# Performance work log

Measured on AMD Instinct MI355X. Metric: run time of the kernel, lower is better.

Reference implementation:

```python
import jax, jax.numpy as jnp
import numpy as np

N = 131072      # total nodes across batched graphs
E = 524288      # total directed edges (avg degree 4, molecular graphs)
F_NODE = 64     # raw atom features
F_BOND = 16     # raw bond features
D = 128         # hidden width (hard-coded in the module)
H2 = 16
G = 4096        # number of graphs in the batch
DIM_OUT = 1


def _make_params(key):
    ks = iter(jax.random.split(key, 64))
    def w(shape, scale):
        return jax.random.normal(next(ks), shape, jnp.float32) * scale
    p = {"fc1_w": w((F_NODE, D), 0.1), "fc1_b": jnp.zeros((D,), jnp.float32)}
    for l in (1, 2, 3):
        p[f"gc{l}_wq"] = w((D, D), 0.05); p[f"gc{l}_bq"] = jnp.zeros((D,), jnp.float32)
        p[f"gc{l}_wk"] = w((D, D), 0.05); p[f"gc{l}_bk"] = jnp.zeros((D,), jnp.float32)
        p[f"gc{l}_wv"] = w((D, D), 0.05); p[f"gc{l}_bv"] = jnp.zeros((D,), jnp.float32)
        p[f"gc{l}_we"] = w((F_BOND, D), 0.05)   # PyG lin_edge has no bias
        p[f"gc{l}_ws"] = w((D, D), 0.05); p[f"gc{l}_bs"] = jnp.zeros((D,), jnp.float32)
    p["fc2_w"] = w((D, H2), 0.1); p["fc2_b"] = jnp.zeros((H2,), jnp.float32)
    p["fc3_w"] = w((H2, DIM_OUT), 0.1); p["fc3_b"] = jnp.zeros((DIM_OUT,), jnp.float32)
    return p


def setup_inputs() -> dict:
    key = jax.random.key(0)
    k1, k2, k3, k4, kp = jax.random.split(key, 5)
    inp = {
        "x": jax.random.normal(k1, (N, F_NODE), jnp.float32),
        "edge_index": jax.random.randint(k2, (2, E), 0, N),
        "edge_attr": jax.random.normal(k3, (E, F_BOND), jnp.float32),
        "batch": jnp.sort(jax.random.randint(k4, (N,), 0, G)),
    }
    inp.update(_make_params(kp))
    return inp


def _tconv(x, src, dst, edge_attr, wq, bq, wk, bk, wv, bv, we, ws, bs):
    # PyG TransformerConv, heads=1, concat=True, beta=False, root_weight=True
    n = x.shape[0]
    q = x @ wq + bq                                   # [N,D]
    k = x @ wk + bk                                   # [N,D]
    v = x @ wv + bv                                   # [N,D]
    e = edge_attr @ we                                # [E,D] edge projection
    kj = k[src] + e                                   # key_j + edge
    vj = v[src] + e                                   # value_j + edge
    alpha = jnp.sum(q[dst] * kj, axis=-1) / jnp.sqrt(jnp.float32(D))   # [E]
    # segment softmax over incoming edges of each dst node
    amax = jax.ops.segment_max(alpha, dst, num_segments=n)
    ex = jnp.exp(alpha - amax[dst])
    denom = jax.ops.segment_sum(ex, dst, num_segments=n)
    w = ex / denom[dst]                               # [E]
    agg = jax.ops.segment_sum(vj * w[:, None], dst, num_segments=n)    # scatter-add
    return agg + x @ ws + bs                          # skip / root weight


def reference(x, edge_index, edge_attr, batch,
              fc1_w, fc1_b,
              gc1_wq, gc1_bq, gc1_wk, gc1_bk, gc1_wv, gc1_bv, gc1_we, gc1_ws, gc1_bs,
              gc2_wq, gc2_bq, gc2_wk, gc2_bk, gc2_wv, gc2_bv, gc2_we, gc2_ws, gc2_bs,
              gc3_wq, gc3_bq, gc3_wk, gc3_bk, gc3_wv, gc3_bv, gc3_we, gc3_ws, gc3_bs,
              fc2_w, fc2_b, fc3_w, fc3_b):
    src, dst = edge_index[0], edge_index[1]
    h = x @ fc1_w + fc1_b
    layers = [
        (gc1_wq, gc1_bq, gc1_wk, gc1_bk, gc1_wv, gc1_bv, gc1_we, gc1_ws, gc1_bs),
        (gc2_wq, gc2_bq, gc2_wk, gc2_bk, gc2_wv, gc2_bv, gc2_we, gc2_ws, gc2_bs),
        (gc3_wq, gc3_bq, gc3_wk, gc3_bk, gc3_wv, gc3_bv, gc3_we, gc3_ws, gc3_bs),
    ]
    for p in layers:
        h = jax.nn.relu(_tconv(h, src, dst, edge_attr, *p))
    # global mean pool over graph ids
    cnt = jax.ops.segment_sum(jnp.ones((h.shape[0],), h.dtype), batch, num_segments=G)
    hg = jax.ops.segment_sum(h, batch, num_segments=G) / jnp.maximum(cnt, 1.0)[:, None]
    h = jax.nn.relu(hg @ fc2_w + fc2_b)
    return h @ fc3_w + fc3_b                          # [G, DIM_OUT]
```

## Files before the change

kernel.cpp:

```cpp
#include <hip/hip_runtime.h>
#include <hip/hip_fp16.h>


#define D 128

typedef _Float16 half8 __attribute__((ext_vector_type(8)));
typedef float f32x4 __attribute__((ext_vector_type(4)));

__global__ __launch_bounds__(256) void hist_kernel(const int* __restrict__ dst,
                                                   int* __restrict__ counts, int e) {
  int i = blockIdx.x * 256 + threadIdx.x;
  if (i < e) atomicAdd(&counts[dst[i]], 1);
}

__global__ __launch_bounds__(256) void scan_a_kernel(const int* __restrict__ counts,
                                                     int* __restrict__ incl,
                                                     int* __restrict__ bsum) {
  int gid = blockIdx.x * 256 + threadIdx.x;
  int lane = threadIdx.x & 63, wid = threadIdx.x >> 6;
  int v = counts[gid];
  int s = v;
  #pragma unroll
  for (int off = 1; off < 64; off <<= 1) {
    int t = __shfl_up(s, off, 64);
    if (lane >= off) s += t;
  }
  __shared__ int wsum[4];
  if (lane == 63) wsum[wid] = s;
  __syncthreads();
  #pragma unroll
  for (int w = 0; w < 3; ++w)
    if (wid > w) s += wsum[w];
  incl[gid] = s;
  if (threadIdx.x == 255) bsum[blockIdx.x] = s;
}

__global__ __launch_bounds__(512) void scan_b_kernel(int* __restrict__ bs) {
  int tid = threadIdx.x;
  int lane = tid & 63, wid = tid >> 6;
  int v = bs[tid];
  int s = v;
  #pragma unroll
  for (int off = 1; off < 64; off <<= 1) {
    int t = __shfl_up(s, off, 64);
    if (lane >= off) s += t;
  }
  __shared__ int wsum[8];
  if (lane == 63) wsum[wid] = s;
  __syncthreads();
  #pragma unroll
  for (int w = 0; w < 7; ++w)
    if (wid > w) s += wsum[w];
  bs[tid] = s - v;
}

__global__ __launch_bounds__(256) void scan_c_kernel(const int* __restrict__ incl,
                                                     const int* __restrict__ counts,
                                                     const int* __restrict__ bsum,
                                                     int* __restrict__ offs, int n, int e) {
  int gid = blockIdx.x * 256 + threadIdx.x;
  if (gid < n) offs[gid] = incl[gid] - counts[gid] + bsum[blockIdx.x];
  if (gid == 0) offs[n] = e;
}

__global__ __launch_bounds__(256) void scatter_kernel(const int* __restrict__ srcs,
                                                      const int* __restrict__ dsts,
                                                      const int* __restrict__ offs,
                                                      int* __restrict__ cursor,
                                                      int* __restrict__ csr_src,
                                                      int* __restrict__ csr_eid, int e) {
  int i = blockIdx.x * 256 + threadIdx.x;
  if (i >= e) return;
  int d = dsts[i];
  int slot = atomicAdd(&cursor[d], 1);
  int p = offs[d] + slot;
  csr_src[p] = srcs[i];
  csr_eid[p] = i;
}

__global__ __launch_bounds__(256) void sort_kernel(const int* __restrict__ offs,
                                                   int* __restrict__ eid,
                                                   int* __restrict__ srcs, int n) {
  int i = blockIdx.x * 256 + threadIdx.x;
  if (i >= n) return;
  int b = offs[i], e = offs[i + 1];
  for (int p = b + 1; p < e; ++p) {
    int ke = eid[p], ks = srcs[p];
    int q = p - 1;
    while (q >= b && eid[q] > ke) {
      eid[q + 1] = eid[q]; srcs[q + 1] = srcs[q]; --q;
    }
    eid[q + 1] = ke; srcs[q + 1] = ks;
  }
}

__global__ __launch_bounds__(256) void convw_kernel(const float* __restrict__ W,
                                                    __half* __restrict__ out,
                                                    int ncols, int K) {
  int idx = blockIdx.x * 256 + threadIdx.x;
  if (idx >= ncols * K) return;
  int n = idx / K, kk = idx - n * K;
  out[idx] = __float2half(W[(size_t)kk * ncols + n]);
}

__global__ __launch_bounds__(256) void bcat_kernel(const float* __restrict__ bq,
                                                   const float* __restrict__ bk,
                                                   const float* __restrict__ bv,
                                                   const float* __restrict__ bs,
                                                   float* __restrict__ out) {
  int j = blockIdx.x * 256 + threadIdx.x;
  if (j >= 512) return;
  const float* src = (j < 128) ? bq : (j < 256) ? bk : (j < 384) ? bv : bs;
  out[j] = src[j & 127];
}

__device__ inline void store4h(__half* p, float4 v) {
  __half2 h01 = __floats2half2_rn(v.x, v.y);
  __half2 h23 = __floats2half2_rn(v.z, v.w);
  uint2 u;
  u.x = *(unsigned int*)&h01;
  u.y = *(unsigned int*)&h23;
  *(uint2*)p = u;
}

template <int K, int NCT, bool QKVS>
__global__ __launch_bounds__(256) void mfma_gemm_kernel(
    const float* in, const __half* __restrict__ Wt, const float* __restrict__ bias,
    __half* __restrict__ oq, __half* __restrict__ ok, __half* __restrict__ ov,
    float* os) {
  constexpr int WST = K + 8;
  __shared__ alignas(16) __half Wc[128 * WST];
  const int tid = threadIdx.x;
  const int w = tid >> 6, l = tid & 63;
  const int lo = l & 15, hi = l >> 4;
  const size_t row = (size_t)blockIdx.x * 64 + w * 16 + lo;

  half8 af[K / 32];
  #pragma unroll
  for (int s = 0; s < K / 32; ++s) {
    const float* sp = in + row * K + s * 32 + hi * 8;
    float4 f0 = *(const float4*)sp;
    float4 f1 = *(const float4*)(sp + 4);
    half8 a;
    a[0] = (_Float16)f0.x; a[1] = (_Float16)f0.y; a[2] = (_Float16)f0.z; a[3] = (_Float16)f0.w;
    a[4] = (_Float16)f1.x; a[5] = (_Float16)f1.y; a[6] = (_Float16)f1.z; a[7] = (_Float16)f1.w;
    af[s] = a;
  }

  #pragma unroll 1
  for (int ch = 0; ch < NCT / 8; ++ch) {
    __syncthreads();
    #pragma unroll
    for (int i = 0; i < 128 * K / 8 / 256; ++i) {
      int idx = i * 256 + tid;
      int col = idx / (K / 8), kk = (idx % (K / 8)) * 8;
      *(uint4*)&Wc[col * WST + kk] =
          *(const uint4*)(Wt + (size_t)(ch * 128 + col) * K + kk);
    }
    __syncthreads();

    #pragma unroll
    for (int t = 0; t < 8; ++t) {
      f32x4 c = {0.f, 0.f, 0.f, 0.f};
      #pragma unroll
      for (int s = 0; s < K / 32; ++s) {
        half8 bf = *(const half8*)&Wc[(t * 16 + lo) * WST + s * 32 + hi * 8];
        c = __builtin_amdgcn_mfma_f32_16x16x32_f16(bf, af[s], c, 0, 0, 0);
      }
      const int col0 = ch * 128 + t * 16 + hi * 4;
      float4 b4 = *(const float4*)(bias + col0);
      float4 o;
      o.x = c[0] + b4.x; o.y = c[1] + b4.y; o.z = c[2] + b4.z; o.w = c[3] + b4.w;
      if (QKVS) {
        const int mid = col0 >> 7, cc = col0 & 127;
        if (mid == 0)      store4h(oq + row * 128 + cc, o);
        else if (mid == 1) store4h(ok + row * 128 + cc, o);
        else if (mid == 2) store4h(ov + row * 128 + cc, o);
        else               *(float4*)(os + row * 128 + cc) = o;
      } else {
        *(float4*)(os + row * 128 + col0) = o;
      }
    }
  }
}

__global__ __launch_bounds__(256) void node_kernel(
    const __half* __restrict__ q, const __half* __restrict__ k, const __half* __restrict__ v,
    float* __restrict__ h, const float* __restrict__ edge_attr,
    const float* __restrict__ we,
    const int* __restrict__ offs, const int* __restrict__ csr_src,
    const int* __restrict__ csr_eid) {
  const int wid = threadIdx.x >> 6, lane = threadIdx.x & 63;
  const int node = __builtin_amdgcn_readfirstlane(blockIdx.x * 4 + wid);
  const int c0 = lane * 2;
  const float inv_sqrt_d = 0.08838834764831845f;

  float2 wreg[16];
  #pragma unroll
  for (int f = 0; f < 16; ++f)
    wreg[f] = *(const float2*)(we + f * D + c0);

  float2 qv = __half22float2(((const __half2*)q)[(size_t)node * 64 + lane]);
  qv.x *= inv_sqrt_d; qv.y *= inv_sqrt_d;
  float2 sv = *(const float2*)(h + (size_t)node * D + c0);

  const int eb = offs[node], ee = offs[node + 1];
  float m = -3.0e38f, den = 0.f, accx = 0.f, accy = 0.f;

  float4 a0n = {0,0,0,0}, a1n = {0,0,0,0}, a2n = {0,0,0,0}, a3n = {0,0,0,0};
  float2 kvn = {0.f, 0.f}, vvn = {0.f, 0.f};
  int p = eb;
  if (p < ee) {
    int src = __builtin_amdgcn_readfirstlane(csr_src[p]);
    int eid = __builtin_amdgcn_readfirstlane(csr_eid[p]);
    const float* ea = edge_attr + (size_t)eid * 16;
    a0n = *(const float4*)(ea + 0);  a1n = *(const float4*)(ea + 4);
    a2n = *(const float4*)(ea + 8);  a3n = *(const float4*)(ea + 12);
    kvn = __half22float2(((const __half2*)k)[(size_t)src * 64 + lane]);
    vvn = __half22float2(((const __half2*)v)[(size_t)src * 64 + lane]);
  }
  while (p < ee) {
    float4 a0 = a0n, a1 = a1n, a2 = a2n, a3 = a3n;
    float2 kv = kvn, vv = vvn;
    ++p;
    if (p < ee) {
      int src = __builtin_amdgcn_readfirstlane(csr_src[p]);
      int eid = __builtin_amdgcn_readfirstlane(csr_eid[p]);
      const float* ea = edge_attr + (size_t)eid * 16;
      a0n = *(const float4*)(ea + 0);  a1n = *(const float4*)(ea + 4);
      a2n = *(const float4*)(ea + 8);  a3n = *(const float4*)(ea + 12);
      kvn = __half22float2(((const __half2*)k)[(size_t)src * 64 + lane]);
      vvn = __half22float2(((const __half2*)v)[(size_t)src * 64 + lane]);
    }
    float ea16[16] = {a0.x, a0.y, a0.z, a0.w, a1.x, a1.y, a1.z, a1.w,
                      a2.x, a2.y, a2.z, a2.w, a3.x, a3.y, a3.z, a3.w};
    float evx = 0.f, evy = 0.f;
    #pragma unroll
    for (int f = 0; f < 16; ++f) {
      evx += ea16[f] * wreg[f].x;
      evy += ea16[f] * wreg[f].y;
    }
    float pa = qv.x * (kv.x + evx) + qv.y * (kv.y + evy);
    #pragma unroll
    for (int off = 32; off > 0; off >>= 1) pa += __shfl_xor(pa, off, 64);
    float vjx = vv.x + evx, vjy = vv.y + evy;
    float mn = fmaxf(m, pa);
    float esc = __expf(m - mn);
    float ew = __expf(pa - mn);
    den = den * esc + ew;
    accx = accx * esc + ew * vjx;
    accy = accy * esc + ew * vjy;
    m = mn;
  }
  if (den > 0.f) {
    sv.x += accx / den;
    sv.y += accy / den;
  }
  sv.x = fmaxf(sv.x, 0.f);
  sv.y = fmaxf(sv.y, 0.f);
  *(float2*)(h + (size_t)node * D + c0) = sv;
}

__global__ __launch_bounds__(64) void pool_kernel(const float* __restrict__ h,
                                                  const int* __restrict__ batch,
                                                  float* __restrict__ hg,
                                                  float* __restrict__ cnt, int n) {
  int base = blockIdx.x * 128;
  int lane = threadIdx.x;
  float2 acc = {0.f, 0.f};
  float run = 0.f;
  int cur = batch[base];
  for (int i = 0; i < 128; ++i) {
    int node = base + i;
    int g = batch[node];
    if (g != cur) {
      atomicAdd(&hg[(size_t)cur * D + 2 * lane], acc.x);
      atomicAdd(&hg[(size_t)cur * D + 2 * lane + 1], acc.y);
      if (lane == 0) atomicAdd(&cnt[cur], run);
      acc.x = acc.y = 0.f; run = 0.f; cur = g;
    }
    float2 hv = *(const float2*)(h + (size_t)node * D + 2 * lane);
    acc.x += hv.x; acc.y += hv.y; run += 1.f;
  }
  atomicAdd(&hg[(size_t)cur * D + 2 * lane], acc.x);
  atomicAdd(&hg[(size_t)cur * D + 2 * lane + 1], acc.y);
  if (lane == 0) atomicAdd(&cnt[cur], run);
}

__global__ __launch_bounds__(256) void head_kernel(const float* __restrict__ hg,
                                                   const float* __restrict__ cnt,
                                                   const float* __restrict__ w2,
                                                   const float* __restrict__ b2,
                                                   const float* __restrict__ w3,
                                                   const float* __restrict__ b3,
                                                   float* __restrict__ out) {
  __shared__ float w2s[128 * 16];
  __shared__ float rowb[4][128];
  for (int i = threadIdx.x; i < (128 * 16) / 4; i += 256)
    ((float4*)w2s)[i] = ((const float4*)w2)[i];
  int wid = threadIdx.x >> 6, lane = threadIdx.x & 63;
  int g = blockIdx.x * 4 + wid;
  float inv = 1.0f / fmaxf(cnt[g], 1.0f);
  rowb[wid][lane] = hg[(size_t)g * D + lane] * inv;
  rowb[wid][lane + 64] = hg[(size_t)g * D + 64 + lane] * inv;
  __syncthreads();
  float t = 0.f;
  if (lane < 16) {
    float a = b2[lane];
    for (int d = 0; d < 128; ++d) a += rowb[wid][d] * w2s[d * 16 + lane];
    t = fmaxf(a, 0.f) * w3[lane];
  }
  #pragma unroll
  for (int off = 8; off > 0; off >>= 1) t += __shfl_xor(t, off, 64);
  if (lane == 0) out[g] = t + b3[0];
}

extern "C" void kernel_launch(void* const* d_in, const int* in_sizes, int n_in,
                              void* d_out, int out_size, void* d_ws, size_t ws_size,
                              hipStream_t stream) {
  const float* x = (const float*)d_in[0];
  const int* eidx = (const int*)d_in[1];
  const float* eattr = (const float*)d_in[2];
  const int* batch = (const int*)d_in[3];
  const float* fc1_w = (const float*)d_in[4];
  const float* fc1_b = (const float*)d_in[5];
  const float* WQ[3] = {(const float*)d_in[6], (const float*)d_in[15], (const float*)d_in[24]};
  const float* BQ[3] = {(const float*)d_in[7], (const float*)d_in[16], (const float*)d_in[25]};
  const float* WK[3] = {(const float*)d_in[8], (const float*)d_in[17], (const float*)d_in[26]};
  const float* BK[3] = {(const float*)d_in[9], (const float*)d_in[18], (const float*)d_in[27]};
  const float* WV[3] = {(const float*)d_in[10], (const float*)d_in[19], (const float*)d_in[28]};
  const float* BV[3] = {(const float*)d_in[11], (const float*)d_in[20], (const float*)d_in[29]};
  const float* WE[3] = {(const float*)d_in[12], (const float*)d_in[21], (const float*)d_in[30]};
  const float* WS[3] = {(const float*)d_in[13], (const float*)d_in[22], (const float*)d_in[31]};
  const float* BS[3] = {(const float*)d_in[14], (const float*)d_in[23], (const float*)d_in[32]};
  const float* fc2_w = (const float*)d_in[33];
  const float* fc2_b = (const float*)d_in[34];
  const float* fc3_w = (const float*)d_in[35];
  const float* fc3_b = (const float*)d_in[36];

  const int N = in_sizes[0] / 64;
  const int E = in_sizes[1] / 2;
  const int G = out_size;
  const int* srcs = eidx;
  const int* dsts = eidx + E;
  const size_t ND = (size_t)N * D;

  char* base = (char*)d_ws;
  size_t off = 0;
  auto alloc = [&](size_t bytes) {
    void* p = base + off;
    off = (off + bytes + 255) & ~(size_t)255;
    return p;
  };
  float* hg = (float*)alloc((size_t)G * D * 4);
  float* cntf = (float*)alloc((size_t)G * 4);
  int* counts = (int*)alloc((size_t)N * 4);
  int* cursor = (int*)alloc((size_t)N * 4);
  size_t zero_bytes = (size_t)G * D * 4 + (size_t)G * 4 + 2 * (size_t)N * 4;
  int* incl = (int*)alloc((size_t)N * 4);
  int* offs = (int*)alloc((size_t)(N + 4) * 4);
  int* bsum = (int*)alloc(512 * 4);
  int* csr_src = (int*)alloc((size_t)E * 4);
  int* csr_eid = (int*)alloc((size_t)E * 4);
  float* h = (float*)alloc(ND * 4);
  __half* q = (__half*)alloc(ND * 2);
  __half* k = (__half*)alloc(ND * 2);
  __half* v = (__half*)alloc(ND * 2);
  __half* Wt[3];
  float* bc[3];
  for (int l = 0; l < 3; ++l) {
    Wt[l] = (__half*)alloc(512 * 128 * 2);
    bc[l] = (float*)alloc(512 * 4);
  }
  __half* fc1t = (__half*)alloc(128 * 64 * 2);
  if (off > ws_size) return;

  hipMemsetAsync(hg, 0, zero_bytes, stream);

  for (int l = 0; l < 3; ++l) {
    convw_kernel<<<64, 256, 0, stream>>>(WQ[l], Wt[l] + 0 * 16384, 128, 128);
    convw_kernel<<<64, 256, 0, stream>>>(WK[l], Wt[l] + 1 * 16384, 128, 128);
    convw_kernel<<<64, 256, 0, stream>>>(WV[l], Wt[l] + 2 * 16384, 128, 128);
    convw_kernel<<<64, 256, 0, stream>>>(WS[l], Wt[l] + 3 * 16384, 128, 128);
    bcat_kernel<<<2, 256, 0, stream>>>(BQ[l], BK[l], BV[l], BS[l], bc[l]);
  }
  convw_kernel<<<32, 256, 0, stream>>>(fc1_w, fc1t, 128, 64);

  hist_kernel<<<E / 256, 256, 0, stream>>>(dsts, counts, E);
  scan_a_kernel<<<N / 256, 256, 0, stream>>>(counts, incl, bsum);
  scan_b_kernel<<<1, 512, 0, stream>>>(bsum);
  scan_c_kernel<<<N / 256, 256, 0, stream>>>(incl, counts, bsum, offs, N, E);
  scatter_kernel<<<E / 256, 256, 0, stream>>>(srcs, dsts, offs, cursor, csr_src, csr_eid, E);
  sort_kernel<<<N / 256, 256, 0, stream>>>(offs, csr_eid, csr_src, N);

  mfma_gemm_kernel<64, 8, false><<<N / 64, 256, 0, stream>>>(
      x, fc1t, fc1_b, nullptr, nullptr, nullptr, h);

  for (int l = 0; l < 3; ++l) {
    mfma_gemm_kernel<128, 32, true><<<N / 64, 256, 0, stream>>>(
        h, Wt[l], bc[l], q, k, v, h);
    node_kernel<<<N / 4, 256, 0, stream>>>(q, k, v, h, eattr, WE[l],
                                           offs, csr_src, csr_eid);
  }

  pool_kernel<<<N / 128, 64, 0, stream>>>(h, batch, hg, cntf, N);
  head_kernel<<<G / 4, 256, 0, stream>>>(hg, cntf, fc2_w, fc2_b, fc3_w, fc3_b, (float*)d_out);
}
```

Baseline: 654.7 us.

## Fold edge projection into query-side precompute and defer edge value projection

Result: slower. 705.7 us (+7.8%).

```diff
diff --git a/kernel.cpp b/kernel.cpp
--- a/kernel.cpp
+++ b/kernel.cpp
@@ -103,6 +103,25 @@
   out[idx] = __float2half(W[(size_t)kk * ncols + n]);
 }
 
+__global__ __launch_bounds__(256) void convwe_kernel(const float* __restrict__ we,
+                                                     const float* __restrict__ Wq,
+                                                     const float* __restrict__ bq,
+                                                     __half* __restrict__ outW,
+                                                     float* __restrict__ outB) {
+  int idx = blockIdx.x * 256 + threadIdx.x;
+  if (idx < 2048) {
+    int f = idx >> 7, kk = idx & 127;
+    float s = 0.f;
+    for (int d = 0; d < 128; ++d) s += we[f * 128 + d] * Wq[kk * 128 + d];
+    outW[f * 128 + kk] = __float2half(s);
+  } else if (idx < 2064) {
+    int f = idx - 2048;
+    float s = 0.f;
+    for (int d = 0; d < 128; ++d) s += we[f * 128 + d] * bq[d];
+    outB[f] = s;
+  }
+}
+
 __global__ __launch_bounds__(256) void bcat_kernel(const float* __restrict__ bq,
                                                    const float* __restrict__ bk,
                                                    const float* __restrict__ bv,
@@ -127,7 +146,7 @@
 __global__ __launch_bounds__(256) void mfma_gemm_kernel(
     const float* in, const __half* __restrict__ Wt, const float* __restrict__ bias,
     __half* __restrict__ oq, __half* __restrict__ ok, __half* __restrict__ ov,
-    float* os) {
+    float* os, float* __restrict__ qt) {
   constexpr int WST = K + 8;
   __shared__ alignas(16) __half Wc[128 * WST];
   const int tid = threadIdx.x;
@@ -182,12 +201,33 @@
       }
     }
   }
+
+  if constexpr (QKVS) {
+    __syncthreads();
+    {
+      int col = tid >> 4;
+      int kk = (tid & 15) * 8;
+      *(uint4*)&Wc[col * WST + kk] =
+          *(const uint4*)(Wt + (size_t)(512 + col) * K + kk);
+    }
+    __syncthreads();
+    f32x4 c = {0.f, 0.f, 0.f, 0.f};
+    #pragma unroll
+    for (int s = 0; s < K / 32; ++s) {
+      half8 bf = *(const half8*)&Wc[lo * WST + s * 32 + hi * 8];
+      c = __builtin_amdgcn_mfma_f32_16x16x32_f16(bf, af[s], c, 0, 0, 0);
+    }
+    float4 b4 = *(const float4*)(bias + 512 + hi * 4);
+    float4 o;
+    o.x = c[0] + b4.x; o.y = c[1] + b4.y; o.z = c[2] + b4.z; o.w = c[3] + b4.w;
+    *(float4*)(qt + row * 16 + hi * 4) = o;
+  }
 }
 
 __global__ __launch_bounds__(256) void node_kernel(
     const __half* __restrict__ q, const __half* __restrict__ k, const __half* __restrict__ v,
     float* __restrict__ h, const float* __restrict__ edge_attr,
-    const float* __restrict__ we,
+    const float* __restrict__ we, const float* __restrict__ tq,
     const int* __restrict__ offs, const int* __restrict__ csr_src,
     const int* __restrict__ csr_eid) {
   const int wid = threadIdx.x >> 6, lane = threadIdx.x & 63;
@@ -201,60 +241,57 @@
     wreg[f] = *(const float2*)(we + f * D + c0);
 
   float2 qv = __half22float2(((const __half2*)q)[(size_t)node * 64 + lane]);
-  qv.x *= inv_sqrt_d; qv.y *= inv_sqrt_d;
   float2 sv = *(const float2*)(h + (size_t)node * D + c0);
+  const float tf = (lane < 16) ? tq[(size_t)node * 16 + lane] : 0.f;
 
   const int eb = offs[node], ee = offs[node + 1];
-  float m = -3.0e38f, den = 0.f, accx = 0.f, accy = 0.f;
-
-  float4 a0n = {0,0,0,0}, a1n = {0,0,0,0}, a2n = {0,0,0,0}, a3n = {0,0,0,0};
+  float m = -3.0e38f, den = 0.f, accx = 0.f, accy = 0.f, accE = 0.f;
+
+  float eafn = 0.f;
   float2 kvn = {0.f, 0.f}, vvn = {0.f, 0.f};
   int p = eb;
   if (p < ee) {
     int src = __builtin_amdgcn_readfirstlane(csr_src[p]);
     int eid = __builtin_amdgcn_readfirstlane(csr_eid[p]);
-    const float* ea = edge_attr + (size_t)eid * 16;
-    a0n = *(const float4*)(ea + 0);  a1n = *(const float4*)(ea + 4);
-    a2n = *(const float4*)(ea + 8);  a3n = *(const float4*)(ea + 12);
+    eafn = (lane < 16) ? edge_attr[(size_t)eid * 16 + lane] : 0.f;
     kvn = __half22float2(((const __half2*)k)[(size_t)src * 64 + lane]);
     vvn = __half22float2(((const __half2*)v)[(size_t)src * 64 + lane]);
   }
   while (p < ee) {
-    float4 a0 = a0n, a1 = a1n, a2 = a2n, a3 = a3n;
+    float eaf = eafn;
     float2 kv = kvn, vv = vvn;
     ++p;
     if (p < ee) {
       int src = __builtin_amdgcn_readfirstlane(csr_src[p]);
       int eid = __builtin_amdgcn_readfirstlane(csr_eid[p]);
-      const float* ea = edge_attr + (size_t)eid * 16;
-      a0n = *(const float4*)(ea + 0);  a1n = *(const float4*)(ea + 4);
-      a2n = *(const float4*)(ea + 8);  a3n = *(const float4*)(ea + 12);
+      eafn = (lane < 16) ? edge_attr[(size_t)eid * 16 + lane] : 0.f;
       kvn = __half22float2(((const __half2*)k)[(size_t)src * 64 + lane]);
       vvn = __half22float2(((const __half2*)v)[(size_t)src * 64 + lane]);
     }
-    float ea16[16] = {a0.x, a0.y, a0.z, a0.w, a1.x, a1.y, a1.z, a1.w,
-                      a2.x, a2.y, a2.z, a2.w, a3.x, a3.y, a3.z, a3.w};
-    float evx = 0.f, evy = 0.f;
-    #pragma unroll
-    for (int f = 0; f < 16; ++f) {
-      evx += ea16[f] * wreg[f].x;
-      evy += ea16[f] * wreg[f].y;
-    }
-    float pa = qv.x * (kv.x + evx) + qv.y * (kv.y + evy);
+    float pa = qv.x * kv.x + qv.y * kv.y + eaf * tf;
     #pragma unroll
     for (int off = 32; off > 0; off >>= 1) pa += __shfl_xor(pa, off, 64);
-    float vjx = vv.x + evx, vjy = vv.y + evy;
+    pa *= inv_sqrt_d;
     float mn = fmaxf(m, pa);
     float esc = __expf(m - mn);
     float ew = __expf(pa - mn);
     den = den * esc + ew;
-    accx = accx * esc + ew * vjx;
-    accy = accy * esc + ew * vjy;
+    accx = accx * esc + ew * vv.x;
+    accy = accy * esc + ew * vv.y;
+    accE = accE * esc + ew * eaf;
     m = mn;
   }
   if (den > 0.f) {
-    sv.x += accx / den;
-    sv.y += accy / den;
+    float inv = 1.0f / den;
+    float ex = 0.f, ey = 0.f;
+    #pragma unroll
+    for (int f = 0; f < 16; ++f) {
+      float aE = __shfl(accE, f, 64);
+      ex += aE * wreg[f].x;
+      ey += aE * wreg[f].y;
+    }
+    sv.x += (accx + ex) * inv;
+    sv.y += (accy + ey) * inv;
   }
   sv.x = fmaxf(sv.x, 0.f);
   sv.y = fmaxf(sv.y, 0.f);
@@ -366,11 +403,12 @@
   __half* q = (__half*)alloc(ND * 2);
   __half* k = (__half*)alloc(ND * 2);
   __half* v = (__half*)alloc(ND * 2);
+  float* qt = (float*)alloc((size_t)N * 16 * 4);
   __half* Wt[3];
   float* bc[3];
   for (int l = 0; l < 3; ++l) {
-    Wt[l] = (__half*)alloc(512 * 128 * 2);
-    bc[l] = (float*)alloc(512 * 4);
+    Wt[l] = (__half*)alloc(528 * 128 * 2);
+    bc[l] = (float*)alloc(544 * 4);
   }
   __half* fc1t = (__half*)alloc(128 * 64 * 2);
   if (off > ws_size) return;
@@ -382,6 +420,8 @@
     convw_kernel<<<64, 256, 0, stream>>>(WK[l], Wt[l] + 1 * 16384, 128, 128);
     convw_kernel<<<64, 256, 0, stream>>>(WV[l], Wt[l] + 2 * 16384, 128, 128);
     convw_kernel<<<64, 256, 0, stream>>>(WS[l], Wt[l] + 3 * 16384, 128, 128);
+    convwe_kernel<<<9, 256, 0, stream>>>(WE[l], WQ[l], BQ[l],
+                                         Wt[l] + 4 * 16384, bc[l] + 512);
     bcat_kernel<<<2, 256, 0, stream>>>(BQ[l], BK[l], BV[l], BS[l], bc[l]);
   }
   convw_kernel<<<32, 256, 0, stream>>>(fc1_w, fc1t, 128, 64);
@@ -394,12 +434,12 @@
   sort_kernel<<<N / 256, 256, 0, stream>>>(offs, csr_eid, csr_src, N);
 
   mfma_gemm_kernel<64, 8, false><<<N / 64, 256, 0, stream>>>(
-      x, fc1t, fc1_b, nullptr, nullptr, nullptr, h);
+      x, fc1t, fc1_b, nullptr, nullptr, nullptr, h, nullptr);
 
   for (int l = 0; l < 3; ++l) {
     mfma_gemm_kernel<128, 32, true><<<N / 64, 256, 0, stream>>>(
-        h, Wt[l], bc[l], q, k, v, h);
-    node_kernel<<<N / 4, 256, 0, stream>>>(q, k, v, h, eattr, WE[l],
+        h, Wt[l], bc[l], q, k, v, h, qt);
+    node_kernel<<<N / 4, 256, 0, stream>>>(q, k, v, h, eattr, WE[l], qt,
                                            offs, csr_src, csr_eid);
   }
 
```
